# Kernel tuning notes

Measured on AMD Instinct MI355X. Metric: run time of the kernel, lower is better.

The kernel has to match this reference:

```python
import jax, jax.numpy as jnp
import numpy as np
from jax import lax


def _laplacian(x):
    # 5-point stencil with edge-replicated (clamped) neighbors, matching
    # F.pad(..., mode='replicate') on shifted slices in the torch code.
    left = jnp.concatenate([x[..., :1], x[..., :-1]], axis=-1)
    right = jnp.concatenate([x[..., 1:], x[..., -1:]], axis=-1)
    up = jnp.concatenate([x[..., :1, :], x[..., :-1, :]], axis=-2)
    down = jnp.concatenate([x[..., 1:, :], x[..., -1:, :]], axis=-2)
    return left + right + up + down - 4.0 * x


def setup_inputs() -> dict:
    key = jax.random.key(0)
    k1, k2, k3 = jax.random.split(key, 3)
    B, M, H, W = 8, 4, 1024, 1024
    initial = jax.random.normal(k1, (B, M, H, W), dtype=jnp.float32)
    diffusion_rates = jnp.ones((M,), dtype=jnp.float32) * 0.1
    decay_rates = jnp.ones((M,), dtype=jnp.float32) * 0.01
    return {"initial": initial, "diffusion_rates": diffusion_rates,
            "decay_rates": decay_rates, "steps": 10}


def reference(initial, diffusion_rates, decay_rates, steps):
    d = diffusion_rates[None, :, None, None]  # [1,M,1,1]
    k = decay_rates[None, :, None, None]

    def body(c, _):
        lap = _laplacian(c)
        return c + d * lap - k * c, None

    conc, _ = lax.scan(body, initial, None, length=steps)
    return conc
```

## Files before the change

### kernel.cpp

```cpp
#include <hip/hip_runtime.h>

constexpr int Hv = 1024, Wv = 1024;
constexpr int TILE   = 64;
constexpr int HALO_R = 10;
constexpr int CHALO  = 16;
constexpr int COLS   = TILE + 2*CHALO;
constexpr int NSTRIP = 32;
constexpr int XPITCH = 100;
constexpr int STEPS  = 10;

__device__ __forceinline__ float4 upd4(const float4 c, const float4 u, const float4 d,
                                       const float lf, const float rt,
                                       const float dif, const float cdec)
{
    float4 o;
    o.x = fmaf(cdec, c.x, dif * ((lf  + c.y) + (u.x + d.x)));
    o.y = fmaf(cdec, c.y, dif * ((c.x + c.z) + (u.y + d.y)));
    o.z = fmaf(cdec, c.z, dif * ((c.y + c.w) + (u.z + d.z)));
    o.w = fmaf(cdec, c.w, dif * ((c.z + rt ) + (u.w + d.w)));
    return o;
}

__device__ __forceinline__ float4 ldrow4(const float* __restrict__ rowp, int gc)
{
    if (gc < 0)        { float e = rowp[0];      return make_float4(e, e, e, e); }
    if (gc > Wv - 4)   { float e = rowp[Wv - 1]; return make_float4(e, e, e, e); }
    return *(const float4*)(rowp + gc);
}

__device__ __forceinline__ void rowupd(const float4& P0, const float4& P1, const float4& P2,
                                       const float4& U0, const float4& U1, const float4& U2,
                                       const float4& D0, const float4& D1, const float4& D2,
                                       bool lclamp, bool rclamp, float dif, float cdec,
                                       float4& O0, float4& O1, float4& O2)
{
    float lv = __shfl_up(P2.w, 1);
    float rv = __shfl_down(P0.x, 1);
    float lA = lclamp ? P1.x : P0.w;
    float rA = rclamp ? P1.w : P2.x;
    O0 = upd4(P0, U0, D0, lv,   P1.x, dif, cdec);
    O1 = upd4(P1, U1, D1, lA,   rA,   dif, cdec);
    O2 = upd4(P2, U2, D2, P1.w, rv,   dif, cdec);
}

__global__ __launch_bounds__(256, 4)
void morpho_reg(const float* __restrict__ src, float* __restrict__ dst,
                const float* __restrict__ dr,  const float* __restrict__ kr)
{
    __shared__ float xtop[NSTRIP * XPITCH];
    __shared__ float xbot[NSTRIP * XPITCH];

    const int b  = blockIdx.x;
    const int bx = b & 15, by = (b >> 4) & 15, plane = b >> 8;
    const float dif  = dr[plane & 3];
    const float dec  = kr[plane & 3];
    const float cdec = 1.0f - 4.0f * dif - dec;
    const int r0 = by * TILE, c0 = bx * TILE;
    const int tid = threadIdx.x;
    const int h = tid & 7;
    const int s = tid >> 3;

    const float* sp = src + ((size_t)plane << 20);

    float4 A0, A1, A2, B0, B1, B2, C0, C1, C2;
    {
        const int rb = r0 - HALO_R + 3 * s;
        const int cb = c0 - CHALO + 12 * h;
        const float* rp0 = sp + ((size_t)min(max(rb    , 0), Hv - 1) << 10);
        const float* rp1 = sp + ((size_t)min(max(rb + 1, 0), Hv - 1) << 10);
        const float* rp2 = sp + ((size_t)min(max(rb + 2, 0), Hv - 1) << 10);
        A0 = ldrow4(rp0, cb); A1 = ldrow4(rp0, cb + 4); A2 = ldrow4(rp0, cb + 8);
        B0 = ldrow4(rp1, cb); B1 = ldrow4(rp1, cb + 4); B2 = ldrow4(rp1, cb + 8);
        C0 = ldrow4(rp2, cb); C1 = ldrow4(rp2, cb + 4); C2 = ldrow4(rp2, cb + 8);
    }

    float*       wt = &xtop[s * XPITCH + 12 * h];
    float*       wb = &xbot[s * XPITCH + 12 * h];
    const float* ru = &xbot[max(s - 1, 0)          * XPITCH + 12 * h];
    const float* rd = &xtop[min(s + 1, NSTRIP - 1) * XPITCH + 12 * h];

    const bool lclamp = (bx == 0)  && (h == 1);
    const bool rclamp = (bx == 15) && (h == 6);
    const bool tclamp = (by == 0)  && (s == 3);
    const bool bclamp = (by == 15) && (s == 24);

    #pragma unroll
    for (int t = 0; t < STEPS; ++t) {
        *(float4*)(wt + 0) = A0; *(float4*)(wt + 4) = A1; *(float4*)(wt + 8) = A2;
        *(float4*)(wb + 0) = C0; *(float4*)(wb + 4) = C1; *(float4*)(wb + 8) = C2;
        __syncthreads();
        float4 U0 = *(const float4*)(ru + 0), U1 = *(const float4*)(ru + 4), U2 = *(const float4*)(ru + 8);
        float4 D0 = *(const float4*)(rd + 0), D1 = *(const float4*)(rd + 4), D2 = *(const float4*)(rd + 8);
        __syncthreads();

        float4 MU0 = tclamp ? B0 : A0, MU1 = tclamp ? B1 : A1, MU2 = tclamp ? B2 : A2;
        float4 MD0 = bclamp ? B0 : C0, MD1 = bclamp ? B1 : C1, MD2 = bclamp ? B2 : C2;

        float4 N10, N11, N12;
        rowupd(B0, B1, B2, MU0, MU1, MU2, MD0, MD1, MD2, lclamp, rclamp, dif, cdec, N10, N11, N12);
        float4 N00, N01, N02;
        rowupd(A0, A1, A2, U0, U1, U2, B0, B1, B2, lclamp, rclamp, dif, cdec, N00, N01, N02);
        float4 N20, N21, N22;
        rowupd(C0, C1, C2, B0, B1, B2, D0, D1, D2, lclamp, rclamp, dif, cdec, N20, N21, N22);

        A0 = N00; A1 = N01; A2 = N02;
        B0 = N10; B1 = N11; B2 = N12;
        C0 = N20; C1 = N21; C2 = N22;
    }

    float* dp = dst + ((size_t)plane << 20);
    const int cbase = 12 * h - CHALO;

#define STORE_ROW(LR, P0, P1, P2) do {                                              \
        const int lr_ = (LR);                                                       \
        if (lr_ >= HALO_R && lr_ < HALO_R + TILE) {                                 \
            float* rp_ = dp + ((size_t)(r0 + lr_ - HALO_R) << 10) + c0;             \
            if (cbase     >= 0 && cbase     <= TILE - 4) *(float4*)(rp_ + cbase)     = P0; \
            if (cbase + 4 >= 0 && cbase + 4 <= TILE - 4) *(float4*)(rp_ + cbase + 4) = P1; \
            if (cbase + 8 >= 0 && cbase + 8 <= TILE - 4) *(float4*)(rp_ + cbase + 8) = P2; \
        } } while (0)

    STORE_ROW(3 * s + 0, A0, A1, A2);
    STORE_ROW(3 * s + 1, B0, B1, B2);
    STORE_ROW(3 * s + 2, C0, C1, C2);
#undef STORE_ROW
}

extern "C" void kernel_launch(void* const* d_in, const int* in_sizes, int n_in,
                              void* d_out, int out_size, void* d_ws, size_t ws_size,
                              hipStream_t stream) {
    const float* init = (const float*)d_in[0];
    const float* dr   = (const float*)d_in[1];
    const float* kr   = (const float*)d_in[2];
    float* out = (float*)d_out;
    morpho_reg<<<dim3(16 * 16 * 32), dim3(256), 0, stream>>>(init, out, dr, kr);
}
```

Before: 321.9 us.

## Replace LDS row exchange with wave shuffles and 12-row register tiles

The kernel now runs one 64-lane wavefront per block, with each lane holding a 12×12 sub-tile in registers instead of 3 rows. Vertical halo rows now move between lanes with cross-lane shuffles (offset 8) rather than through shared memory. This removes both LDS round-trips and both __syncthreads barriers per time step. In exchange each thread carries far more live registers (a 12×3 float4 array plus temporaries), which lowers occupancy and risks spills. The time loop is no longer unrolled.

```diff
diff --git a/kernel.cpp b/kernel.cpp
--- a/kernel.cpp
+++ b/kernel.cpp
@@ -4,9 +4,7 @@
 constexpr int TILE   = 64;
 constexpr int HALO_R = 10;
 constexpr int CHALO  = 16;
-constexpr int COLS   = TILE + 2*CHALO;
-constexpr int NSTRIP = 32;
-constexpr int XPITCH = 100;
+constexpr int RPL    = 12;
 constexpr int STEPS  = 10;
 
 __device__ __forceinline__ float4 upd4(const float4 c, const float4 u, const float4 d,
@@ -28,28 +26,21 @@
     return *(const float4*)(rowp + gc);
 }
 
-__device__ __forceinline__ void rowupd(const float4& P0, const float4& P1, const float4& P2,
-                                       const float4& U0, const float4& U1, const float4& U2,
-                                       const float4& D0, const float4& D1, const float4& D2,
-                                       bool lclamp, bool rclamp, float dif, float cdec,
-                                       float4& O0, float4& O1, float4& O2)
+__device__ __forceinline__ float4 shflup4(const float4 v, int d)
 {
-    float lv = __shfl_up(P2.w, 1);
-    float rv = __shfl_down(P0.x, 1);
-    float lA = lclamp ? P1.x : P0.w;
-    float rA = rclamp ? P1.w : P2.x;
-    O0 = upd4(P0, U0, D0, lv,   P1.x, dif, cdec);
-    O1 = upd4(P1, U1, D1, lA,   rA,   dif, cdec);
-    O2 = upd4(P2, U2, D2, P1.w, rv,   dif, cdec);
+    return make_float4(__shfl_up(v.x, d), __shfl_up(v.y, d),
+                       __shfl_up(v.z, d), __shfl_up(v.w, d));
+}
+__device__ __forceinline__ float4 shfldn4(const float4 v, int d)
+{
+    return make_float4(__shfl_down(v.x, d), __shfl_down(v.y, d),
+                       __shfl_down(v.z, d), __shfl_down(v.w, d));
 }
 
-__global__ __launch_bounds__(256, 4)
-void morpho_reg(const float* __restrict__ src, float* __restrict__ dst,
-                const float* __restrict__ dr,  const float* __restrict__ kr)
+__global__ __launch_bounds__(64, 2)
+void morpho_wave(const float* __restrict__ src, float* __restrict__ dst,
+                 const float* __restrict__ dr,  const float* __restrict__ kr)
 {
-    __shared__ float xtop[NSTRIP * XPITCH];
-    __shared__ float xbot[NSTRIP * XPITCH];
-
     const int b  = blockIdx.x;
     const int bx = b & 15, by = (b >> 4) & 15, plane = b >> 8;
     const float dif  = dr[plane & 3];
@@ -62,68 +53,67 @@
 
     const float* sp = src + ((size_t)plane << 20);
 
-    float4 A0, A1, A2, B0, B1, B2, C0, C1, C2;
+    float4 T[RPL][3];
     {
-        const int rb = r0 - HALO_R + 3 * s;
+        const int rb = r0 - HALO_R + RPL * s;
         const int cb = c0 - CHALO + 12 * h;
-        const float* rp0 = sp + ((size_t)min(max(rb    , 0), Hv - 1) << 10);
-        const float* rp1 = sp + ((size_t)min(max(rb + 1, 0), Hv - 1) << 10);
-        const float* rp2 = sp + ((size_t)min(max(rb + 2, 0), Hv - 1) << 10);
-        A0 = ldrow4(rp0, cb); A1 = ldrow4(rp0, cb + 4); A2 = ldrow4(rp0, cb + 8);
-        B0 = ldrow4(rp1, cb); B1 = ldrow4(rp1, cb + 4); B2 = ldrow4(rp1, cb + 8);
-        C0 = ldrow4(rp2, cb); C1 = ldrow4(rp2, cb + 4); C2 = ldrow4(rp2, cb + 8);
+        #pragma unroll
+        for (int i = 0; i < RPL; ++i) {
+            const float* rp = sp + ((size_t)min(max(rb + i, 0), Hv - 1) << 10);
+            T[i][0] = ldrow4(rp, cb);
+            T[i][1] = ldrow4(rp, cb + 4);
+            T[i][2] = ldrow4(rp, cb + 8);
+        }
     }
-
-    float*       wt = &xtop[s * XPITCH + 12 * h];
-    float*       wb = &xbot[s * XPITCH + 12 * h];
-    const float* ru = &xbot[max(s - 1, 0)          * XPITCH + 12 * h];
-    const float* rd = &xtop[min(s + 1, NSTRIP - 1) * XPITCH + 12 * h];
 
     const bool lclamp = (bx == 0)  && (h == 1);
     const bool rclamp = (bx == 15) && (h == 6);
-    const bool tclamp = (by == 0)  && (s == 3);
-    const bool bclamp = (by == 15) && (s == 24);
+    const bool tclamp = (by == 0)  && (s == 0);
+    const bool bclamp = (by == 15) && (s == 6);
 
-    #pragma unroll
+    #pragma unroll 1
     for (int t = 0; t < STEPS; ++t) {
-        *(float4*)(wt + 0) = A0; *(float4*)(wt + 4) = A1; *(float4*)(wt + 8) = A2;
-        *(float4*)(wb + 0) = C0; *(float4*)(wb + 4) = C1; *(float4*)(wb + 8) = C2;
-        __syncthreads();
-        float4 U0 = *(const float4*)(ru + 0), U1 = *(const float4*)(ru + 4), U2 = *(const float4*)(ru + 8);
-        float4 D0 = *(const float4*)(rd + 0), D1 = *(const float4*)(rd + 4), D2 = *(const float4*)(rd + 8);
-        __syncthreads();
+        float4 U0 = shflup4(T[RPL-1][0], 8), U1 = shflup4(T[RPL-1][1], 8), U2 = shflup4(T[RPL-1][2], 8);
+        float4 D0 = shfldn4(T[0][0], 8),     D1 = shfldn4(T[0][1], 8),     D2 = shfldn4(T[0][2], 8);
 
-        float4 MU0 = tclamp ? B0 : A0, MU1 = tclamp ? B1 : A1, MU2 = tclamp ? B2 : A2;
-        float4 MD0 = bclamp ? B0 : C0, MD1 = bclamp ? B1 : C1, MD2 = bclamp ? B2 : C2;
-
-        float4 N10, N11, N12;
-        rowupd(B0, B1, B2, MU0, MU1, MU2, MD0, MD1, MD2, lclamp, rclamp, dif, cdec, N10, N11, N12);
-        float4 N00, N01, N02;
-        rowupd(A0, A1, A2, U0, U1, U2, B0, B1, B2, lclamp, rclamp, dif, cdec, N00, N01, N02);
-        float4 N20, N21, N22;
-        rowupd(C0, C1, C2, B0, B1, B2, D0, D1, D2, lclamp, rclamp, dif, cdec, N20, N21, N22);
-
-        A0 = N00; A1 = N01; A2 = N02;
-        B0 = N10; B1 = N11; B2 = N12;
-        C0 = N20; C1 = N21; C2 = N22;
+        float4 P0 = U0, P1 = U1, P2 = U2;
+        #pragma unroll
+        for (int i = 0; i < RPL; ++i) {
+            const float4 a  = T[i][0], b4 = T[i][1], c4 = T[i][2];
+            float4 d0, d1, d2;
+            if (i < RPL - 1) { d0 = T[i+1][0]; d1 = T[i+1][1]; d2 = T[i+1][2]; }
+            else             { d0 = D0;        d1 = D1;        d2 = D2;        }
+            float4 u0 = P0, u1 = P1, u2 = P2;
+            if (i == 10) {
+                u0 = tclamp ? a : u0; u1 = tclamp ? b4 : u1; u2 = tclamp ? c4 : u2;
+            }
+            if (i == 1) {
+                d0 = bclamp ? a : d0; d1 = bclamp ? b4 : d1; d2 = bclamp ? c4 : d2;
+            }
+            float lv = __shfl_up(c4.w, 1);
+            float rv = __shfl_down(a.x, 1);
+            float lA = lclamp ? b4.x : a.w;
+            float rA = rclamp ? b4.w : c4.x;
+            float4 n0 = upd4(a,  u0, d0, lv,   b4.x, dif, cdec);
+            float4 n1 = upd4(b4, u1, d1, lA,   rA,   dif, cdec);
+            float4 n2 = upd4(c4, u2, d2, b4.w, rv,   dif, cdec);
+            P0 = a; P1 = b4; P2 = c4;
+            T[i][0] = n0; T[i][1] = n1; T[i][2] = n2;
+        }
     }
 
     float* dp = dst + ((size_t)plane << 20);
     const int cbase = 12 * h - CHALO;
-
-#define STORE_ROW(LR, P0, P1, P2) do {                                              \
-        const int lr_ = (LR);                                                       \
-        if (lr_ >= HALO_R && lr_ < HALO_R + TILE) {                                 \
-            float* rp_ = dp + ((size_t)(r0 + lr_ - HALO_R) << 10) + c0;             \
-            if (cbase     >= 0 && cbase     <= TILE - 4) *(float4*)(rp_ + cbase)     = P0; \
-            if (cbase + 4 >= 0 && cbase + 4 <= TILE - 4) *(float4*)(rp_ + cbase + 4) = P1; \
-            if (cbase + 8 >= 0 && cbase + 8 <= TILE - 4) *(float4*)(rp_ + cbase + 8) = P2; \
-        } } while (0)
-
-    STORE_ROW(3 * s + 0, A0, A1, A2);
-    STORE_ROW(3 * s + 1, B0, B1, B2);
-    STORE_ROW(3 * s + 2, C0, C1, C2);
-#undef STORE_ROW
+    #pragma unroll
+    for (int i = 0; i < RPL; ++i) {
+        const int lr = RPL * s + i;
+        if (lr >= HALO_R && lr < HALO_R + TILE) {
+            float* rp_ = dp + ((size_t)(r0 + lr - HALO_R) << 10) + c0;
+            if (cbase     >= 0 && cbase     <= TILE - 4) *(float4*)(rp_ + cbase)     = T[i][0];
+            if (cbase + 4 >= 0 && cbase + 4 <= TILE - 4) *(float4*)(rp_ + cbase + 4) = T[i][1];
+            if (cbase + 8 >= 0 && cbase + 8 <= TILE - 4) *(float4*)(rp_ + cbase + 8) = T[i][2];
+        }
+    }
 }
 
 extern "C" void kernel_launch(void* const* d_in, const int* in_sizes, int n_in,
@@ -133,5 +123,5 @@
     const float* dr   = (const float*)d_in[1];
     const float* kr   = (const float*)d_in[2];
     float* out = (float*)d_out;
-    morpho_reg<<<dim3(16 * 16 * 32), dim3(256), 0, stream>>>(init, out, dr, kr);
+    morpho_wave<<<dim3(16 * 16 * 32), dim3(64), 0, stream>>>(init, out, dr, kr);
 }
```

Measured after the change: 879.2 us. +173.1%, slower.

## Exchange vertical halo rows via wave shuffles, using shared memory only across waves

Applied to the files above, without the earlier changes.

The vertical neighbor exchange between row strips now goes through cross-lane shuffles by 8 lanes inside each 64-lane wave. Only the boundary strips of each wave write and read a small double-buffered shared array, so each step needs one barrier instead of two. The time loop is no longer unrolled. This cuts LDS traffic and barrier count but adds many shuffle (ds_bpermute-style) instructions and select logic per step. It also risks extra loop overhead from the loss of unrolling.

```diff
diff --git a/kernel.cpp b/kernel.cpp
--- a/kernel.cpp
+++ b/kernel.cpp
@@ -4,9 +4,6 @@
 constexpr int TILE   = 64;
 constexpr int HALO_R = 10;
 constexpr int CHALO  = 16;
-constexpr int COLS   = TILE + 2*CHALO;
-constexpr int NSTRIP = 32;
-constexpr int XPITCH = 100;
 constexpr int STEPS  = 10;
 
 __device__ __forceinline__ float4 upd4(const float4 c, const float4 u, const float4 d,
@@ -28,27 +25,29 @@
     return *(const float4*)(rowp + gc);
 }
 
-__device__ __forceinline__ void rowupd(const float4& P0, const float4& P1, const float4& P2,
-                                       const float4& U0, const float4& U1, const float4& U2,
-                                       const float4& D0, const float4& D1, const float4& D2,
-                                       bool lclamp, bool rclamp, float dif, float cdec,
-                                       float4& O0, float4& O1, float4& O2)
-{
-    float lv = __shfl_up(P2.w, 1);
-    float rv = __shfl_down(P0.x, 1);
-    float lA = lclamp ? P1.x : P0.w;
-    float rA = rclamp ? P1.w : P2.x;
-    O0 = upd4(P0, U0, D0, lv,   P1.x, dif, cdec);
-    O1 = upd4(P1, U1, D1, lA,   rA,   dif, cdec);
-    O2 = upd4(P2, U2, D2, P1.w, rv,   dif, cdec);
-}
+__device__ __forceinline__ float4 shflup4(const float4 v, int d)
+{ return make_float4(__shfl_up(v.x,d),__shfl_up(v.y,d),__shfl_up(v.z,d),__shfl_up(v.w,d)); }
+__device__ __forceinline__ float4 shfldn4(const float4 v, int d)
+{ return make_float4(__shfl_down(v.x,d),__shfl_down(v.y,d),__shfl_down(v.z,d),__shfl_down(v.w,d)); }
+__device__ __forceinline__ float4 sel4(bool p, const float4 a, const float4 b)
+{ float4 o; o.x=p?a.x:b.x; o.y=p?a.y:b.y; o.z=p?a.z:b.z; o.w=p?a.w:b.w; return o; }
+
+#define ROWUPD(Pa,Pb,Pc, Ua,Ub,Uc, Xa,Xb,Xc, Oa,Ob,Oc) do {            \
+    float lv_ = __shfl_up((Pc).w, 1);           \
+    float rv_ = __shfl_down((Pa).x, 1);       \
+    float lA_ = lclamp ? (Pb).x : (Pa).w;    \
+    float rA_ = rclamp ? (Pb).w : (Pc).x;       \
+    Oa = upd4((Pa), (Ua), (Xa), lv_, (Pb).x, dif, cdec);               \
+    Ob = upd4((Pb), (Ub), (Xb), lA_, rA_,    dif, cdec);               \
+    Oc = upd4((Pc), (Uc), (Xc), (Pb).w, rv_, dif, cdec);               \
+} while (0)
 
 __global__ __launch_bounds__(256, 4)
-void morpho_reg(const float* __restrict__ src, float* __restrict__ dst,
-                const float* __restrict__ dr,  const float* __restrict__ kr)
+void morpho_shfl(const float* __restrict__ src, float* __restrict__ dst,
+                 const float* __restrict__ dr,  const float* __restrict__ kr)
 {
-    __shared__ float xtop[NSTRIP * XPITCH];
-    __shared__ float xbot[NSTRIP * XPITCH];
+    __shared__ float4 xbot[2][4][24];
+    __shared__ float4 xtop[2][4][24];
 
     const int b  = blockIdx.x;
     const int bx = b & 15, by = (b >> 4) & 15, plane = b >> 8;
@@ -59,70 +58,79 @@
     const int tid = threadIdx.x;
     const int h = tid & 7;
     const int s = tid >> 3;
+    const int w = tid >> 6;
 
     const float* sp = src + ((size_t)plane << 20);
 
-    float4 A0, A1, A2, B0, B1, B2, C0, C1, C2;
+    float4 T0a,T0b,T0c, T1a,T1b,T1c, T2a,T2b,T2c;
     {
         const int rb = r0 - HALO_R + 3 * s;
         const int cb = c0 - CHALO + 12 * h;
         const float* rp0 = sp + ((size_t)min(max(rb    , 0), Hv - 1) << 10);
         const float* rp1 = sp + ((size_t)min(max(rb + 1, 0), Hv - 1) << 10);
         const float* rp2 = sp + ((size_t)min(max(rb + 2, 0), Hv - 1) << 10);
-        A0 = ldrow4(rp0, cb); A1 = ldrow4(rp0, cb + 4); A2 = ldrow4(rp0, cb + 8);
-        B0 = ldrow4(rp1, cb); B1 = ldrow4(rp1, cb + 4); B2 = ldrow4(rp1, cb + 8);
-        C0 = ldrow4(rp2, cb); C1 = ldrow4(rp2, cb + 4); C2 = ldrow4(rp2, cb + 8);
+        T0a = ldrow4(rp0, cb); T0b = ldrow4(rp0, cb + 4); T0c = ldrow4(rp0, cb + 8);
+        T1a = ldrow4(rp1, cb); T1b = ldrow4(rp1, cb + 4); T1c = ldrow4(rp1, cb + 8);
+        T2a = ldrow4(rp2, cb); T2b = ldrow4(rp2, cb + 4); T2c = ldrow4(rp2, cb + 8);
     }
-
-    float*       wt = &xtop[s * XPITCH + 12 * h];
-    float*       wb = &xbot[s * XPITCH + 12 * h];
-    const float* ru = &xbot[max(s - 1, 0)          * XPITCH + 12 * h];
-    const float* rd = &xtop[min(s + 1, NSTRIP - 1) * XPITCH + 12 * h];
 
     const bool lclamp = (bx == 0)  && (h == 1);
     const bool rclamp = (bx == 15) && (h == 6);
     const bool tclamp = (by == 0)  && (s == 3);
     const bool bclamp = (by == 15) && (s == 24);
+    const bool isBot  = ((s & 7) == 7);
+    const bool isTop  = ((s & 7) == 0);
+    const bool dsel   = isBot && (w < 3);
+    const bool usel   = isTop && (w > 0);
+    const int  wp = min(w + 1, 3), wm = max(w - 1, 0);
 
-    #pragma unroll
+    int par = 0;
+    #pragma unroll 1
     for (int t = 0; t < STEPS; ++t) {
-        *(float4*)(wt + 0) = A0; *(float4*)(wt + 4) = A1; *(float4*)(wt + 8) = A2;
-        *(float4*)(wb + 0) = C0; *(float4*)(wb + 4) = C1; *(float4*)(wb + 8) = C2;
-        __syncthreads();
-        float4 U0 = *(const float4*)(ru + 0), U1 = *(const float4*)(ru + 4), U2 = *(const float4*)(ru + 8);
-        float4 D0 = *(const float4*)(rd + 0), D1 = *(const float4*)(rd + 4), D2 = *(const float4*)(rd + 8);
+        float4 Da = shfldn4(T0a, 8), Db = shfldn4(T0b, 8), Dc = shfldn4(T0c, 8);
+
+        if (isBot) { xbot[par][w][3*h+0] = T2a; xbot[par][w][3*h+1] = T2b; xbot[par][w][3*h+2] = T2c; }
+        if (isTop) { xtop[par][w][3*h+0] = T0a; xtop[par][w][3*h+1] = T0b; xtop[par][w][3*h+2] = T0c; }
         __syncthreads();
 
-        float4 MU0 = tclamp ? B0 : A0, MU1 = tclamp ? B1 : A1, MU2 = tclamp ? B2 : A2;
-        float4 MD0 = bclamp ? B0 : C0, MD1 = bclamp ? B1 : C1, MD2 = bclamp ? B2 : C2;
+        {
+            float4 qa = xtop[par][wp][3*h+0], qb = xtop[par][wp][3*h+1], qc = xtop[par][wp][3*h+2];
+            Da = sel4(dsel, qa, Da); Db = sel4(dsel, qb, Db); Dc = sel4(dsel, qc, Dc);
+        }
+        float4 Ua = shflup4(T2a, 8), Ub = shflup4(T2b, 8), Uc = shflup4(T2c, 8);
+        {
+            float4 ra = xbot[par][wm][3*h+0], rb4 = xbot[par][wm][3*h+1], rc = xbot[par][wm][3*h+2];
+            Ua = sel4(usel, ra, Ua); Ub = sel4(usel, rb4, Ub); Uc = sel4(usel, rc, Uc);
+        }
 
-        float4 N10, N11, N12;
-        rowupd(B0, B1, B2, MU0, MU1, MU2, MD0, MD1, MD2, lclamp, rclamp, dif, cdec, N10, N11, N12);
-        float4 N00, N01, N02;
-        rowupd(A0, A1, A2, U0, U1, U2, B0, B1, B2, lclamp, rclamp, dif, cdec, N00, N01, N02);
-        float4 N20, N21, N22;
-        rowupd(C0, C1, C2, B0, B1, B2, D0, D1, D2, lclamp, rclamp, dif, cdec, N20, N21, N22);
-
-        A0 = N00; A1 = N01; A2 = N02;
-        B0 = N10; B1 = N11; B2 = N12;
-        C0 = N20; C1 = N21; C2 = N22;
+        float4 n0a, n0b, n0c;
+        ROWUPD(T0a,T0b,T0c, Ua,Ub,Uc, T1a,T1b,T1c, n0a,n0b,n0c);
+        float4 u1a = sel4(tclamp, T1a, T0a), u1b = sel4(tclamp, T1b, T0b), u1c = sel4(tclamp, T1c, T0c);
+        float4 d1a = sel4(bclamp, T1a, T2a), d1b = sel4(bclamp, T1b, T2b), d1c = sel4(bclamp, T1c, T2c);
+        float4 n1a, n1b, n1c;
+        ROWUPD(T1a,T1b,T1c, u1a,u1b,u1c, d1a,d1b,d1c, n1a,n1b,n1c);
+        T0a = n0a; T0b = n0b; T0c = n0c;
+        float4 n2a, n2b, n2c;
+        ROWUPD(T2a,T2b,T2c, T1a,T1b,T1c, Da,Db,Dc, n2a,n2b,n2c);
+        T1a = n1a; T1b = n1b; T1c = n1c;
+        T2a = n2a; T2b = n2b; T2c = n2c;
+        par ^= 1;
     }
 
     float* dp = dst + ((size_t)plane << 20);
     const int cbase = 12 * h - CHALO;
-
-#define STORE_ROW(LR, P0, P1, P2) do {                                              \
-        const int lr_ = (LR);                                                       \
-        if (lr_ >= HALO_R && lr_ < HALO_R + TILE) {                                 \
-            float* rp_ = dp + ((size_t)(r0 + lr_ - HALO_R) << 10) + c0;             \
-            if (cbase     >= 0 && cbase     <= TILE - 4) *(float4*)(rp_ + cbase)     = P0; \
-            if (cbase + 4 >= 0 && cbase + 4 <= TILE - 4) *(float4*)(rp_ + cbase + 4) = P1; \
-            if (cbase + 8 >= 0 && cbase + 8 <= TILE - 4) *(float4*)(rp_ + cbase + 8) = P2; \
+#define STORE_ROW(LR, Pa, Pb, Pc) do {                                             \
+        const int lr_ = (LR);                                                      \
+        if (lr_ >= HALO_R && lr_ < HALO_R + TILE) {                                \
+            float* rp_ = dp + ((size_t)(r0 + lr_ - HALO_R) << 10) + c0;            \
+            if (cbase     >= 0 && cbase     <= TILE - 4) *(float4*)(rp_ + cbase)     = Pa; \
+            if (cbase + 4 >= 0 && cbase + 4 <= TILE - 4) *(float4*)(rp_ + cbase + 4) = Pb; \
+            if (cbase + 8 >= 0 && cbase + 8 <= TILE - 4) *(float4*)(rp_ + cbase + 8) = Pc; \
         } } while (0)
 
-    STORE_ROW(3 * s + 0, A0, A1, A2);
-    STORE_ROW(3 * s + 1, B0, B1, B2);
-    STORE_ROW(3 * s + 2, C0, C1, C2);
+    STORE_ROW(3 * s + 0, T0a, T0b, T0c);
+    STORE_ROW(3 * s + 1, T1a, T1b, T1c);
+    STORE_ROW(3 * s + 2, T2a, T2b, T2c);
 #undef STORE_ROW
 }
 
@@ -133,5 +141,5 @@
     const float* dr   = (const float*)d_in[1];
     const float* kr   = (const float*)d_in[2];
     float* out = (float*)d_out;
-    morpho_reg<<<dim3(16 * 16 * 32), dim3(256), 0, stream>>>(init, out, dr, kr);
+    morpho_shfl<<<dim3(16 * 16 * 32), dim3(256), 0, stream>>>(init, out, dr, kr);
 }
```

Result: slower. 350.2 us (+8.8%).
